# Performance work log

Hardware: AMD Instinct MI355X
Metric: run time of the kernel (lower is better)

## Reference

```python
import jax, jax.numpy as jnp
import numpy as np

C, H, W = 8, 2048, 2048
NUM_SEG = 64      # labels 0..63; label 0 = background (ndimage.label convention)
SIGMA_AGG = 0.5


def setup_inputs() -> dict:
    key = jax.random.key(0)
    k1, k2, k3 = jax.random.split(key, 3)
    pred_similarities = jax.random.normal(k1, (C, H, W), dtype=jnp.float32)
    kernel_labels = jax.random.randint(k2, (H, W), 0, NUM_SEG).astype(jnp.int32)
    region_labels = jax.random.randint(k3, (H, W), 0, NUM_SEG).astype(jnp.int32)
    # masks are 1 exactly where a connected component exists (labels > 0),
    # matching what ndimage.label would produce from these masks
    kernels_mask = (kernel_labels > 0).astype(jnp.float32)
    regions_mask = (region_labels > 0).astype(jnp.float32)
    return {
        "pred_similarities": pred_similarities,
        "regions_mask": regions_mask,
        "kernels_mask": kernels_mask,
        "kernel_labels": kernel_labels,
        "region_labels": region_labels,
    }


def reference(pred_similarities, regions_mask, kernels_mask, kernel_labels, region_labels):
    h, w = kernel_labels.shape
    kl = kernel_labels.reshape(-1)  # [N]
    rl = region_labels.reshape(-1)  # [N]

    # per-label cardinality, broadcast back to pixels (label 0 contributes 0
    # because the mask is 0 there, matching the original's untouched zeros)
    kcard = jax.ops.segment_sum(kernels_mask.reshape(-1), kl, num_segments=NUM_SEG)[kl].reshape(h, w)
    rcard = jax.ops.segment_sum(regions_mask.reshape(-1), rl, num_segments=NUM_SEG)[rl].reshape(h, w)

    # per-channel, per-kernel-component sum of pred, broadcast back per pixel
    c = pred_similarities.shape[0]
    pred_flat = pred_similarities.reshape(c, -1)  # [C, N]
    seg = jax.vmap(lambda p: jax.ops.segment_sum(p, kl, num_segments=NUM_SEG))(pred_flat)  # [C, NUM_SEG]
    Gk = jnp.where(kl[None, :] > 0, seg[:, kl], 0.0).reshape(c, h, w)
    Gk = Gk / (kcard + 1.0)[None]

    Fp = pred_similarities * regions_mask[None]
    diff = Fp - Gk
    # torch.linalg.norm over the whole tensor -> scalar Frobenius norm
    D = jnp.maximum(jnp.sqrt(jnp.sum(diff * diff)) - SIGMA_AGG, 0.0)
    per_pixel = jnp.log(D * D + 1.0) / (rcard + 1.0)  # [H, W]

    num_region = jnp.maximum(jnp.max(region_labels), 1).astype(per_pixel.dtype)
    return jnp.sum(per_pixel) / num_region
```

## Files before the change

### kernel.cpp

```cpp
#include <hip/hip_runtime.h>
#include <math.h>

#define NPIX (2048*2048)
#define NGROUPS (NPIX/32)
#define NBLOCKS 1024
#define NWAVES (NBLOCKS*4)

#define WS_FLOATS 3073
#define WS_F2 3072
#define LROW 17
#define LTAB (64*LROW)
#define LDS_FLOATS (3*LTAB)

typedef __attribute__((ext_vector_type(8))) short short8;
typedef __attribute__((ext_vector_type(4))) float f32x4;
typedef __attribute__((ext_vector_type(4))) unsigned int u32x4;

__device__ inline unsigned int pk_trunc_bf16(float lo, float hi) {
    return __builtin_amdgcn_perm(__float_as_uint(hi), __float_as_uint(lo), 0x07060302u);
}
__device__ inline unsigned int pk_lab(int lo, int hi) {
    return __builtin_amdgcn_perm((unsigned)hi, (unsigned)lo, 0x05040100u);
}
__device__ inline unsigned int onehot2(unsigned int x, unsigned int tp) {
    const unsigned int a = x ^ tp;
    const unsigned int t = 0x40004000u - a;
    return t & 0x40004000u;
}

struct GroupBuf {
    int4 ka, kb, ra, rb;
    float4 pa, pb;
};

__device__ inline void load_group(GroupBuf& b, const float* predc,
                                  const int* kl, const int* rl, int g, int quad) {
    const int p8 = g * 32 + quad * 8;
    b.ka = *(const int4*)(kl + p8);
    b.kb = *(const int4*)(kl + p8 + 4);
    b.ra = *(const int4*)(rl + p8);
    b.rb = *(const int4*)(rl + p8 + 4);
    b.pa = *(const float4*)(predc + p8);
    b.pb = *(const float4*)(predc + p8 + 4);
}

__global__ __launch_bounds__(256, 4) void agg_mfma(
    const float* __restrict__ pred,
    const int*   __restrict__ kl,
    const int*   __restrict__ rl,
    float* __restrict__ ws)
{
    const int tid  = threadIdx.x;
    const int wv   = tid >> 6;
    const int lane = tid & 63;
    const int quad = lane >> 4;
    const int col  = lane & 15;
    const int c8   = col & 7;
    const bool lowcol = (col < 8);
    const unsigned int cpack = (unsigned)col * 0x00010001u;
    const unsigned int tps[4] = {cpack, cpack + 0x00100010u,
                                 cpack + 0x00200020u, cpack + 0x00300030u};
    const unsigned int hc = (col == 8) ? 0x3F803F80u : 0u;
    const short8 b2c = __builtin_bit_cast(short8, (u32x4){hc, hc, hc, hc});

    f32x4 acc[12];
    #pragma unroll
    for (int s = 0; s < 12; ++s) acc[s] = (f32x4){0.f, 0.f, 0.f, 0.f};
    float f2 = 0.f;

    const float* predc = pred + (size_t)c8 * NPIX;
    const int gw = blockIdx.x * 4 + wv;

    GroupBuf cur, nxt;
    load_group(cur, predc, kl, rl, gw, quad);

    for (int g = gw; g < NGROUPS; g += NWAVES) {
        const int gn = g + NWAVES;
        load_group(nxt, predc, kl, rl, (gn < NGROUPS) ? gn : gw, quad);

        const int   klv[8] = {cur.ka.x, cur.ka.y, cur.ka.z, cur.ka.w,
                              cur.kb.x, cur.kb.y, cur.kb.z, cur.kb.w};
        const int   rlv[8] = {cur.ra.x, cur.ra.y, cur.ra.z, cur.ra.w,
                              cur.rb.x, cur.rb.y, cur.rb.z, cur.rb.w};
        const float pv[8]  = {cur.pa.x, cur.pa.y, cur.pa.z, cur.pa.w,
                              cur.pb.x, cur.pb.y, cur.pb.z, cur.pb.w};

        float pr[8];
        #pragma unroll
        for (int j = 0; j < 8; ++j) {
            pr[j] = (rlv[j] > 0) ? pv[j] : 0.f;
            f2 = fmaf(pr[j], pr[j], f2);
        }

        unsigned int b1p[4], kp[4], rp[4];
        #pragma unroll
        for (int i = 0; i < 4; ++i) {
            const int j0 = 2 * i, j1 = 2 * i + 1;
            const unsigned int plo = pk_trunc_bf16(pv[j0], pv[j1]);
            const unsigned int phi = pk_trunc_bf16(pr[j0], pr[j1]);
            b1p[i] = lowcol ? plo : phi;
            kp[i]  = pk_lab(klv[j0], klv[j1]);
            rp[i]  = pk_lab(rlv[j0], rlv[j1]);
        }
        const short8 b1 = __builtin_bit_cast(short8, (u32x4){b1p[0], b1p[1], b1p[2], b1p[3]});

        #pragma unroll
        for (int t = 0; t < 4; ++t) {
            u32x4 ohk, ohr;
            #pragma unroll
            for (int i = 0; i < 4; ++i) {
                ohk[i] = onehot2(kp[i], tps[t]);
                ohr[i] = onehot2(rp[i], tps[t]);
            }
            const short8 ak = __builtin_bit_cast(short8, ohk);
            const short8 ar = __builtin_bit_cast(short8, ohr);
            acc[t]     = __builtin_amdgcn_mfma_f32_16x16x32_bf16(ak, b1,  acc[t],     0, 0, 0);
            acc[4 + t] = __builtin_amdgcn_mfma_f32_16x16x32_bf16(ak, b2c, acc[4 + t], 0, 0, 0);
            acc[8 + t] = __builtin_amdgcn_mfma_f32_16x16x32_bf16(ar, b2c, acc[8 + t], 0, 0, 0);
        }

        cur = nxt;
    }

    __shared__ float s_f2w[4];
    #pragma unroll
    for (int off = 32; off > 0; off >>= 1) f2 += __shfl_down(f2, off, 64);
    if (lane == 0) s_f2w[wv] = f2;

    __shared__ float sws[LDS_FLOATS];
    __syncthreads();
    for (int w = 0; w < 4; ++w) {
        if (wv == w) {
            #pragma unroll
            for (int s = 0; s < 12; ++s) {
                const int T = s >> 2, t = s & 3;
                #pragma unroll
                for (int i = 0; i < 4; ++i) {
                    const int l = t * 16 + quad * 4 + i;
                    const int a = T * LTAB + l * LROW + col;
                    if (w == 0) sws[a] = acc[s][i];
                    else        sws[a] += acc[s][i];
                }
            }
        }
        __syncthreads();
    }
    if (tid == 0)
        atomicAdd(&ws[WS_F2], s_f2w[0] + s_f2w[1] + s_f2w[2] + s_f2w[3]);
    for (int idx = tid; idx < 3072; idx += 256) {
        const int T = idx >> 10, r = idx & 1023, l = r >> 4, c = r & 15;
        atomicAdd(&ws[idx], sws[T * LTAB + l * LROW + c]);
    }
}

__global__ __launch_bounds__(64) void agg_final(const float* __restrict__ ws,
                                                float* __restrict__ out)
{
    const int l = threadIdx.x;
    const float* t0 = ws + l * 16;
    const float* t1 = ws + 1024 + l * 16;
    const float* t2 = ws + 2048 + l * 16;

    const float pck = 0.5f * t1[8];
    const float pcr = 0.5f * t2[8];
    float corr = 0.f;
    if (l > 0) {
        #pragma unroll
        for (int c = 0; c < 8; ++c) {
            const float seg = 0.5f * t0[c];
            const float T   = 0.5f * t0[8 + c];
            const float gk  = seg / (pck + 1.f);
            corr += gk * (gk * pck - 2.f * T);
        }
    }
    const float rcard = (l > 0) ? pcr : 0.f;
    float S = pcr / (rcard + 1.f);
    int mx = (pcr > 0.5f) ? l : 0;
    float f2 = (l == 0) ? 0.5f * ws[WS_F2] : 0.f;

    #pragma unroll
    for (int off = 32; off > 0; off >>= 1) {
        f2   += __shfl_down(f2, off, 64);
        corr += __shfl_down(corr, off, 64);
        S    += __shfl_down(S, off, 64);
        mx    = max(mx, __shfl_down(mx, off, 64));
    }
    if (l == 0) {
        const float SS = f2 + corr;
        float D = sqrtf(fmaxf(SS, 0.f)) - 0.5f;
        D = fmaxf(D, 0.f);
        out[0] = logf(D * D + 1.f) * S / (float)max(mx, 1);
    }
}

extern "C" void kernel_launch(void* const* d_in, const int* in_sizes, int n_in,
                              void* d_out, int out_size, void* d_ws, size_t ws_size,
                              hipStream_t stream) {
    const float* pred = (const float*)d_in[0];
    const int* kl = (const int*)d_in[3];
    const int* rl = (const int*)d_in[4];
    float* ws = (float*)d_ws;

    hipMemsetAsync(d_ws, 0, WS_FLOATS * sizeof(float), stream);
    agg_mfma<<<NBLOCKS, 256, 0, stream>>>(pred, kl, rl, ws);
    agg_final<<<1, 64, 0, stream>>>(ws, (float*)d_out);
}
```

Measured before the change: 262.9 us.

## Compute label histograms with single factored one-hot MFMA and unroll main loop

Label counts were previously computed with four MFMAs per table against a constant column. They now use one MFMA per table whose A and B operands are one-hot encodings of the low 4 bits and high 2 bits of each label, which yields a 16x4 count matrix. This cuts MFMA work from 12 to 6 per group and shrinks the LDS and workspace reduction. The main loop is also manually unrolled by two with ping-pong buffers, and the grid and occupancy target are raised to 1280 blocks with 5 waves per SIMD. Risks are register pressure from the higher occupancy target and a wrap-around prefetch via a group mask.

```diff
diff --git a/kernel.cpp b/kernel.cpp
--- a/kernel.cpp
+++ b/kernel.cpp
@@ -3,14 +3,17 @@
 
 #define NPIX (2048*2048)
 #define NGROUPS (NPIX/32)
-#define NBLOCKS 1024
+#define GMASK (NGROUPS-1)
+#define NBLOCKS 1280
 #define NWAVES (NBLOCKS*4)
 
-#define WS_FLOATS 3073
-#define WS_F2 3072
-#define LROW 17
-#define LTAB (64*LROW)
-#define LDS_FLOATS (3*LTAB)
+#define WS_T1 1024
+#define WS_T2 1280
+#define WS_F2 1536
+#define WS_FLOATS 1537
+#define L_T1 1088
+#define L_T2 1360
+#define LDS_FLOATS 1632
 
 typedef __attribute__((ext_vector_type(8))) short short8;
 typedef __attribute__((ext_vector_type(4))) float f32x4;
@@ -44,7 +47,57 @@
     b.pb = *(const float4*)(predc + p8 + 4);
 }
 
-__global__ __launch_bounds__(256, 4) void agg_mfma(
+__device__ inline void compute_group(
+    const GroupBuf& b, float& f2, f32x4 acc0[4], f32x4& acc1, f32x4& acc2,
+    const unsigned int* tps, unsigned int cpack, bool lowcol)
+{
+    const int   klv[8] = {b.ka.x, b.ka.y, b.ka.z, b.ka.w, b.kb.x, b.kb.y, b.kb.z, b.kb.w};
+    const int   rlv[8] = {b.ra.x, b.ra.y, b.ra.z, b.ra.w, b.rb.x, b.rb.y, b.rb.z, b.rb.w};
+    const float pv[8]  = {b.pa.x, b.pa.y, b.pa.z, b.pa.w, b.pb.x, b.pb.y, b.pb.z, b.pb.w};
+
+    float pr[8];
+    #pragma unroll
+    for (int j = 0; j < 8; ++j) {
+        pr[j] = (rlv[j] > 0) ? pv[j] : 0.f;
+        f2 = fmaf(pr[j], pr[j], f2);
+    }
+    unsigned int b1p[4], kp[4], rp[4];
+    #pragma unroll
+    for (int i = 0; i < 4; ++i) {
+        const int j0 = 2 * i, j1 = 2 * i + 1;
+        const unsigned int plo = pk_trunc_bf16(pv[j0], pv[j1]);
+        const unsigned int phi = pk_trunc_bf16(pr[j0], pr[j1]);
+        b1p[i] = lowcol ? plo : phi;
+        kp[i]  = pk_lab(klv[j0], klv[j1]);
+        rp[i]  = pk_lab(rlv[j0], rlv[j1]);
+    }
+    const short8 b1 = __builtin_bit_cast(short8, (u32x4){b1p[0], b1p[1], b1p[2], b1p[3]});
+    #pragma unroll
+    for (int t = 0; t < 4; ++t) {
+        u32x4 oh;
+        #pragma unroll
+        for (int i = 0; i < 4; ++i) oh[i] = onehot2(kp[i], tps[t]);
+        acc0[t] = __builtin_amdgcn_mfma_f32_16x16x32_bf16(
+            __builtin_bit_cast(short8, oh), b1, acc0[t], 0, 0, 0);
+    }
+    u32x4 alo, bhi;
+    #pragma unroll
+    for (int i = 0; i < 4; ++i) {
+        alo[i] = onehot2(kp[i] & 0x000F000Fu, cpack);
+        bhi[i] = onehot2((kp[i] >> 4) & 0x00030003u, cpack);
+    }
+    acc1 = __builtin_amdgcn_mfma_f32_16x16x32_bf16(
+        __builtin_bit_cast(short8, alo), __builtin_bit_cast(short8, bhi), acc1, 0, 0, 0);
+    #pragma unroll
+    for (int i = 0; i < 4; ++i) {
+        alo[i] = onehot2(rp[i] & 0x000F000Fu, cpack);
+        bhi[i] = onehot2((rp[i] >> 4) & 0x00030003u, cpack);
+    }
+    acc2 = __builtin_amdgcn_mfma_f32_16x16x32_bf16(
+        __builtin_bit_cast(short8, alo), __builtin_bit_cast(short8, bhi), acc2, 0, 0, 0);
+}
+
+__global__ __launch_bounds__(256, 5) void agg_mfma(
     const float* __restrict__ pred,
     const int*   __restrict__ kl,
     const int*   __restrict__ rl,
@@ -60,67 +113,28 @@
     const unsigned int cpack = (unsigned)col * 0x00010001u;
     const unsigned int tps[4] = {cpack, cpack + 0x00100010u,
                                  cpack + 0x00200020u, cpack + 0x00300030u};
-    const unsigned int hc = (col == 8) ? 0x3F803F80u : 0u;
-    const short8 b2c = __builtin_bit_cast(short8, (u32x4){hc, hc, hc, hc});
-
-    f32x4 acc[12];
-    #pragma unroll
-    for (int s = 0; s < 12; ++s) acc[s] = (f32x4){0.f, 0.f, 0.f, 0.f};
+
+    f32x4 acc0[4], acc1, acc2;
+    #pragma unroll
+    for (int s = 0; s < 4; ++s) acc0[s] = (f32x4){0.f, 0.f, 0.f, 0.f};
+    acc1 = (f32x4){0.f, 0.f, 0.f, 0.f};
+    acc2 = (f32x4){0.f, 0.f, 0.f, 0.f};
     float f2 = 0.f;
 
     const float* predc = pred + (size_t)c8 * NPIX;
     const int gw = blockIdx.x * 4 + wv;
 
-    GroupBuf cur, nxt;
-    load_group(cur, predc, kl, rl, gw, quad);
-
-    for (int g = gw; g < NGROUPS; g += NWAVES) {
-        const int gn = g + NWAVES;
-        load_group(nxt, predc, kl, rl, (gn < NGROUPS) ? gn : gw, quad);
-
-        const int   klv[8] = {cur.ka.x, cur.ka.y, cur.ka.z, cur.ka.w,
-                              cur.kb.x, cur.kb.y, cur.kb.z, cur.kb.w};
-        const int   rlv[8] = {cur.ra.x, cur.ra.y, cur.ra.z, cur.ra.w,
-                              cur.rb.x, cur.rb.y, cur.rb.z, cur.rb.w};
-        const float pv[8]  = {cur.pa.x, cur.pa.y, cur.pa.z, cur.pa.w,
-                              cur.pb.x, cur.pb.y, cur.pb.z, cur.pb.w};
-
-        float pr[8];
-        #pragma unroll
-        for (int j = 0; j < 8; ++j) {
-            pr[j] = (rlv[j] > 0) ? pv[j] : 0.f;
-            f2 = fmaf(pr[j], pr[j], f2);
-        }
-
-        unsigned int b1p[4], kp[4], rp[4];
-        #pragma unroll
-        for (int i = 0; i < 4; ++i) {
-            const int j0 = 2 * i, j1 = 2 * i + 1;
-            const unsigned int plo = pk_trunc_bf16(pv[j0], pv[j1]);
-            const unsigned int phi = pk_trunc_bf16(pr[j0], pr[j1]);
-            b1p[i] = lowcol ? plo : phi;
-            kp[i]  = pk_lab(klv[j0], klv[j1]);
-            rp[i]  = pk_lab(rlv[j0], rlv[j1]);
-        }
-        const short8 b1 = __builtin_bit_cast(short8, (u32x4){b1p[0], b1p[1], b1p[2], b1p[3]});
-
-        #pragma unroll
-        for (int t = 0; t < 4; ++t) {
-            u32x4 ohk, ohr;
-            #pragma unroll
-            for (int i = 0; i < 4; ++i) {
-                ohk[i] = onehot2(kp[i], tps[t]);
-                ohr[i] = onehot2(rp[i], tps[t]);
-            }
-            const short8 ak = __builtin_bit_cast(short8, ohk);
-            const short8 ar = __builtin_bit_cast(short8, ohr);
-            acc[t]     = __builtin_amdgcn_mfma_f32_16x16x32_bf16(ak, b1,  acc[t],     0, 0, 0);
-            acc[4 + t] = __builtin_amdgcn_mfma_f32_16x16x32_bf16(ak, b2c, acc[4 + t], 0, 0, 0);
-            acc[8 + t] = __builtin_amdgcn_mfma_f32_16x16x32_bf16(ar, b2c, acc[8 + t], 0, 0, 0);
-        }
-
-        cur = nxt;
-    }
+    GroupBuf bA, bB;
+    int g = gw;
+    load_group(bA, predc, kl, rl, g, quad);
+    for (; g + NWAVES < NGROUPS; g += 2 * NWAVES) {
+        load_group(bB, predc, kl, rl, g + NWAVES, quad);
+        compute_group(bA, f2, acc0, acc1, acc2, tps, cpack, lowcol);
+        load_group(bA, predc, kl, rl, (g + 2 * NWAVES) & GMASK, quad);
+        compute_group(bB, f2, acc0, acc1, acc2, tps, cpack, lowcol);
+    }
+    if (g < NGROUPS)
+        compute_group(bA, f2, acc0, acc1, acc2, tps, cpack, lowcol);
 
     __shared__ float s_f2w[4];
     #pragma unroll
@@ -132,24 +146,32 @@
     for (int w = 0; w < 4; ++w) {
         if (wv == w) {
             #pragma unroll
-            for (int s = 0; s < 12; ++s) {
-                const int T = s >> 2, t = s & 3;
+            for (int t = 0; t < 4; ++t)
                 #pragma unroll
                 for (int i = 0; i < 4; ++i) {
                     const int l = t * 16 + quad * 4 + i;
-                    const int a = T * LTAB + l * LROW + col;
-                    if (w == 0) sws[a] = acc[s][i];
-                    else        sws[a] += acc[s][i];
+                    const int a = l * 17 + col;
+                    if (w == 0) sws[a] = acc0[t][i]; else sws[a] += acc0[t][i];
                 }
+            #pragma unroll
+            for (int i = 0; i < 4; ++i) {
+                const int row = quad * 4 + i;
+                const int a1 = L_T1 + row * 17 + col;
+                const int a2 = L_T2 + row * 17 + col;
+                if (w == 0) { sws[a1] = acc1[i]; sws[a2] = acc2[i]; }
+                else        { sws[a1] += acc1[i]; sws[a2] += acc2[i]; }
             }
         }
         __syncthreads();
     }
     if (tid == 0)
         atomicAdd(&ws[WS_F2], s_f2w[0] + s_f2w[1] + s_f2w[2] + s_f2w[3]);
-    for (int idx = tid; idx < 3072; idx += 256) {
-        const int T = idx >> 10, r = idx & 1023, l = r >> 4, c = r & 15;
-        atomicAdd(&ws[idx], sws[T * LTAB + l * LROW + c]);
+    for (int idx = tid; idx < 1536; idx += 256) {
+        int a;
+        if (idx < 1024)      a = (idx >> 4) * 17 + (idx & 15);
+        else if (idx < 1280) a = L_T1 + ((idx - 1024) >> 4) * 17 + (idx & 15);
+        else                 a = L_T2 + ((idx - 1280) >> 4) * 17 + (idx & 15);
+        atomicAdd(&ws[idx], sws[a]);
     }
 }
 
@@ -158,11 +180,9 @@
 {
     const int l = threadIdx.x;
     const float* t0 = ws + l * 16;
-    const float* t1 = ws + 1024 + l * 16;
-    const float* t2 = ws + 2048 + l * 16;
-
-    const float pck = 0.5f * t1[8];
-    const float pcr = 0.5f * t2[8];
+    const float pck = 0.25f * ws[WS_T1 + (l & 15) * 16 + (l >> 4)];
+    const float pcr = 0.25f * ws[WS_T2 + (l & 15) * 16 + (l >> 4)];
+
     float corr = 0.f;
     if (l > 0) {
         #pragma unroll
```

After: 439.2 us. 1.67x slower.
